# Performance work log

Measured on AMD Instinct MI355X. Metric: run time of the kernel, lower is better.

The kernel has to match this reference:

```python
import jax, jax.numpy as jnp
import numpy as np

N = 50000       # nodes
E = 1600000     # edges
H = 64          # hidden_channels
G = 16          # graphs in batch
DOUT = 2        # dim_out
NODE_IN = 1
EDGE_IN = 3


def setup_inputs() -> dict:
    key = jax.random.key(0)
    ks = jax.random.split(key, 24)
    p = lambda k, shape: (jax.random.normal(k, shape, jnp.float32) * 0.05)
    inp = {
        "x": jax.random.normal(ks[0], (N, NODE_IN), jnp.float32),
        "edge_index": jax.random.randint(ks[1], (2, E), 0, N, dtype=jnp.int64),
        "edge_attr": jax.random.normal(ks[2], (E, EDGE_IN), jnp.float32),
        "batch": jnp.sort(jax.random.randint(ks[3], (N,), 0, G, dtype=jnp.int64)),
        # EdgeModel MLP: Linear(2*node_in+edge_in, H), ReLU, Linear(H, H)
        "ew1": p(ks[4], (2 * NODE_IN + EDGE_IN, H)), "eb1": p(ks[5], (H,)),
        "ew2": p(ks[6], (H, H)), "eb2": p(ks[7], (H,)),
        # NodeModel MLP: Linear(node_in+edge_out, H), ReLU, Linear(H, H)
        "nw1": p(ks[8], (NODE_IN + H, H)), "nb1": p(ks[9], (H,)),
        "nw2": p(ks[10], (H, H)), "nb2": p(ks[11], (H,)),
        "ow1": p(ks[12], (H, H)), "ob1": p(ks[13], (H,)),
        "ow2": p(ks[14], (H, H)), "ob2": p(ks[15], (H,)),
        "ow3": p(ks[16], (H, H)), "ob3": p(ks[17], (H,)),
        "ow4": p(ks[18], (H, DOUT)), "ob4": p(ks[19], (DOUT,)),
    }
    return inp


def reference(x, edge_index, edge_attr, batch,
              ew1, eb1, ew2, eb2,
              nw1, nb1, nw2, nb2,
              ow1, ob1, ow2, ob2, ow3, ob3, ow4, ob4):
    row, col = edge_index[0], edge_index[1]
    # EdgeModel: gather endpoints, concat, 2-layer MLP (no residual)
    e_in = jnp.concatenate([x[row], x[col], edge_attr], axis=1)      # [E, 2+3]
    e = jax.nn.relu(e_in @ ew1 + eb1) @ ew2 + eb2                    # [E, H]
    # NodeModel: scatter_add edge messages into destination nodes
    agg = jax.ops.segment_sum(e, col, num_segments=x.shape[0])      # [N, H]
    h_in = jnp.concatenate([x, agg], axis=1)                         # [N, 1+H]
    h = jax.nn.relu(h_in @ nw1 + nb1) @ nw2 + nb2                    # [N, H]
    # global_add_pool over graphs
    pooled = jax.ops.segment_sum(h, batch, num_segments=G)          # [G, H]
    o = jax.nn.relu(pooled @ ow1 + ob1)
    o = jax.nn.relu(o @ ow2 + ob2)
    o = jax.nn.relu(o @ ow3 + ob3)
    return o @ ow4 + ob4                                             # [G, DOUT]
```

## Files before the change

### kernel.cpp

```cpp
#include <hip/hip_runtime.h>
#include <hip/hip_bf16.h>

#define HID 64
#define NGRAPH 16
#define BN 32
#define GB 8
#define MAXNB 2048
#define NCB 256
#define NCT 1024
#define SORT_T 1024
#define SORT_CHUNK 12800

typedef __attribute__((ext_vector_type(8))) short short8;
typedef __attribute__((ext_vector_type(4))) float f32x4;

enum : int {
  OFF_V      = 1040,
  OFF_M      = 1104,
  OFF_EW1    = 5200,
  OFF_EB1    = 5520,
  OFF_NW1    = 5584,
  OFF_NB1    = 9744,
  OFF_NW2    = 9808,
  OFF_NB2    = 13904,
  OFF_OW1    = 13968,
  OFF_OB1    = 18064,
  OFF_OW2    = 18128,
  OFF_OB2    = 22224,
  OFF_OW3    = 22288,
  OFF_OB3    = 26384,
  OFF_OW4    = 26448,
  OFF_OB4    = 26576,
  OFF_EW2    = 26580,
  OFF_EB2    = 30676,
  OFF_FLAGS  = 30740,
  OFF_W1T    = 30744,
  OFF_MT     = 31000,
  OFF_PREP   = 33048
};

struct WPtrs { const void* p[16]; };

__device__ __forceinline__ float cv(float v) { return v; }
__device__ __forceinline__ float cv(__hip_bfloat16 v) { return __bfloat162float(v); }
__device__ __forceinline__ float b2f(unsigned short u) {
  union { unsigned u32; float f; } c;
  c.u32 = ((unsigned)u) << 16;
  return c.f;
}
__device__ __forceinline__ unsigned short f2bu(float v) {
  union { __hip_bfloat16 b; unsigned short u; } c;
  c.b = __float2bfloat16(v);
  return c.u;
}
__device__ __forceinline__ unsigned short fr(float v) {
  unsigned u = __float_as_uint(v);
  u += 0x7FFFu + ((u >> 16) & 1u);
  return (unsigned short)(u >> 16);
}
__device__ __forceinline__ unsigned rndpack(float a, float b) {
  unsigned ua = __float_as_uint(fmaxf(a, 0.0f));
  unsigned ub = __float_as_uint(fmaxf(b, 0.0f));
  ua += 0x7FFFu + ((ua >> 16) & 1u);
  ub += 0x7FFFu + ((ub >> 16) & 1u);
  return __builtin_amdgcn_perm(ub, ua, 0x07060302u);
}

__global__ __launch_bounds__(1024) void prep_kernel(
    const void* xv, const void* eiv, WPtrs wp, float* ws)
{
  __shared__ int red[2];
  __shared__ int s_ft;
  __shared__ float ew2s[4096];
  __shared__ float nw1s[4096];
  const int t = threadIdx.x;
  const int lane = t & 63;

  if (t == 0) { red[0] = 0; red[1] = 0; }
  __syncthreads();
  {
    int big = 0;
    if (t < 512) {
      const unsigned el = (((const unsigned*)xv)[t] >> 7) & 0xFFu;
      big = (el >= 140u) ? 1 : 0;
    }
    #pragma unroll
    for (int o = 32; o > 0; o >>= 1) big += __shfl_xor(big, o);
    if (lane == 0 && big) atomicAdd(&red[0], big);
  }
  {
    int orv = ((const int*)eiv)[1 + 2 * t];
    #pragma unroll
    for (int o = 32; o > 0; o >>= 1) orv |= __shfl_xor(orv, o);
    if (lane == 0 && orv) atomicOr(&red[1], orv);
  }
  __syncthreads();
  if (t == 0) {
    const int ft = (red[0] < 8) ? 1 : 0;
    const int it = (red[1] == 0) ? 1 : 0;
    ((int*)(ws + OFF_FLAGS))[0] = ft;
    ((int*)(ws + OFF_FLAGS))[1] = it;
    s_ft = ft;
  }
  __syncthreads();
  const int ft = s_ft;

  const int sz[16]  = {320,64,4096,64,4160,64,4096,64,4096,64,4096,64,4096,64,128,2};
  const int dst[16] = {OFF_EW1,OFF_EB1,OFF_EW2,OFF_EB2,OFF_NW1,OFF_NB1,OFF_NW2,OFF_NB2,
                       OFF_OW1,OFF_OB1,OFF_OW2,OFF_OB2,OFF_OW3,OFF_OB3,OFF_OW4,OFF_OB4};
  for (int a = 0; a < 16; ++a) {
    const void* src = wp.p[a];
    float* d = ws + dst[a];
    const int n = sz[a];
    const int n4 = n >> 2;
    for (int i = t; i < n4; i += 1024) {
      float4 f;
      if (ft) {
        const ushort4 u4 = ((const ushort4*)src)[i];
        f.x = b2f(u4.x); f.y = b2f(u4.y); f.z = b2f(u4.z); f.w = b2f(u4.w);
      } else {
        f = ((const float4*)src)[i];
      }
      ((float4*)d)[i] = f;
      const int g = i << 2;
      if (a == 2) {
        ew2s[g] = f.x; ew2s[g + 1] = f.y; ew2s[g + 2] = f.z; ew2s[g + 3] = f.w;
      } else if (a == 4 && g >= 64) {
        nw1s[g - 64] = f.x; nw1s[g - 63] = f.y; nw1s[g - 62] = f.z; nw1s[g - 61] = f.w;
      }
    }
    for (int i = (n4 << 2) + t; i < n; i += 1024)
      d[i] = ft ? b2f(((const unsigned short*)src)[i]) : ((const float*)src)[i];
  }
  __syncthreads();

  float mv[4];
  #pragma unroll
  for (int p = 0; p < 4; ++p) {
    const int idx = t + p * 1024;
    const int i = idx >> 6, j = idx & 63;
    float s = 0.0f;
    #pragma unroll 8
    for (int k = 0; k < 64; ++k)
      s = fmaf(ew2s[i * 64 + k], nw1s[k * 64 + j], s);
    mv[p] = s;
  }
  if (t < 64) {
    float s = 0.0f;
    #pragma unroll 8
    for (int k = 0; k < 64; ++k)
      s = fmaf(ws[OFF_EB2 + k], nw1s[k * 64 + t], s);
    ws[OFF_V + t] = s;
  }
  __syncthreads();
  #pragma unroll
  for (int p = 0; p < 4; ++p) ew2s[t + p * 1024] = mv[p];
  __syncthreads();

  if (t < 64) {
    unsigned short* w1t = (unsigned short*)(ws + OFF_W1T);
    #pragma unroll
    for (int k = 0; k < 8; ++k) {
      float v = 0.0f;
      if (k < 5) v = ws[OFF_EW1 + k * 64 + t];
      else if (k == 5) v = ws[OFF_EB1 + t];
      w1t[t * 8 + k] = f2bu(v);
    }
  }
  unsigned short* mt = (unsigned short*)(ws + OFF_MT);
  #pragma unroll
  for (int p = 0; p < 4; ++p) {
    const int idx = t + p * 1024;
    const int n = idx >> 6, k = idx & 63;
    mt[idx] = f2bu(ew2s[k * 64 + n]);
  }
}

template<typename IT>
__device__ __forceinline__ void count_impl(
    const IT* __restrict__ ei, const IT* __restrict__ bt,
    int* __restrict__ gcnt, int* __restrict__ endG, int* lh,
    const int E, const int N, const int NBG)
{
  const int t = threadIdx.x;
  const int b = blockIdx.x;
  for (int i = t; i < NBG; i += NCT) lh[i] = 0;
  {
    const int i = b * NCT + t;
    if (i < N) {
      const int g1 = (int)bt[i];
      if (i == 0) for (int g = 0; g < g1; ++g) endG[g] = 0;
      if (i == N - 1) {
        for (int g = g1; g < NGRAPH; ++g) endG[g] = N;
      } else {
        const int g2 = (int)bt[i + 1];
        for (int g = g1; g < g2; ++g) endG[g] = i + 1;
      }
    }
  }
  __syncthreads();
  const int per = (E + NCB - 1) / NCB;
  const int a = b * per;
  const int bnd = (a + per < E) ? (a + per) : E;
  for (int e = a + t; e < bnd; e += NCT) {
    const int c = (int)ei[(size_t)E + e];
    atomicAdd(&lh[c >> 8], 1);
  }
  __syncthreads();
  for (int i = t; i < NBG; i += NCT) gcnt[(size_t)i * NCB + b] = lh[i];
}

__global__ __launch_bounds__(NCT) void count_kernel(
    const void* eiv, const void* batv, const float* ws,
    int* gcnt, int* endG, const int E, const int N, const int NBG)
{
  __shared__ int lh[MAXNB];
  const int it = ((const int*)(ws + OFF_FLAGS))[1];
  if (it) count_impl<long long>((const long long*)eiv, (const long long*)batv, gcnt, endG, lh, E, N, NBG);
  else    count_impl<int>((const int*)eiv, (const int*)batv, gcnt, endG, lh, E, N, NBG);
}

__global__ __launch_bounds__(256) void scan_tot_kernel(
    const int* __restrict__ gcnt, int* __restrict__ gstart, const int NBG)
{
  const int lane = threadIdx.x & 63;
  const int bkt = blockIdx.x * 4 + (threadIdx.x >> 6);
  if (bkt >= NBG) return;
  const int4 v = *(const int4*)(gcnt + (size_t)bkt * NCB + lane * 4);
  int s = v.x + v.y + v.z + v.w;
  #pragma unroll
  for (int off = 32; off > 0; off >>= 1) s += __shfl_xor(s, off);
  if (lane == 0) gstart[bkt] = s;
}

__global__ __launch_bounds__(256) void scan_pref_kernel(
    int* __restrict__ gstart, const int NBG)
{
  __shared__ int ps[256];
  const int t = threadIdx.x;
  const int seg = (NBG + 255) / 256;
  int s = 0;
  for (int i = 0; i < seg; ++i) {
    const int idx = t * seg + i;
    if (idx < NBG) s += gstart[idx];
  }
  ps[t] = s;
  __syncthreads();
  for (int off = 1; off < 256; off <<= 1) {
    const int v = (t >= off) ? ps[t - off] : 0;
    __syncthreads();
    ps[t] += v;
    __syncthreads();
  }
  int carry = ps[t] - s;
  for (int i = 0; i < seg; ++i) {
    const int idx = t * seg + i;
    if (idx < NBG) {
      const int c = gstart[idx];
      gstart[idx] = carry;
      carry += c;
    }
  }
  if (t == 255) gstart[NBG] = ps[255];
}

__global__ __launch_bounds__(256) void scan_row_kernel(
    int* __restrict__ gcnt, const int* __restrict__ gstart, const int NBG)
{
  const int lane = threadIdx.x & 63;
  const int bkt = blockIdx.x * 4 + (threadIdx.x >> 6);
  if (bkt >= NBG) return;
  int* row = gcnt + (size_t)bkt * NCB;
  const int4 v = *(const int4*)(row + lane * 4);
  const int ls = v.x + v.y + v.z + v.w;
  int s = ls;
  #pragma unroll
  for (int off = 1; off < 64; off <<= 1) {
    const int u = __shfl_up(s, off);
    if (lane >= off) s += u;
  }
  int e = s - ls + gstart[bkt];
  int4 o;
  o.x = e; e += v.x;
  o.y = e; e += v.y;
  o.z = e; e += v.z;
  o.w = e;
  *(int4*)(row + lane * 4) = o;
}

template<typename FT, typename IT>
__device__ __forceinline__ void scatter_impl(
    const FT* __restrict__ x, const IT* __restrict__ ei, const FT* __restrict__ ea,
    const int* __restrict__ gcnt, const int* __restrict__ gstart,
    ushort4* __restrict__ recB, unsigned char* __restrict__ cid, int* lb,
    const int E, const int gb0, const int gb1, const int cap)
{
  const int t = threadIdx.x;
  const int b = blockIdx.x;
  __shared__ int sbase;
  if (t == 0) sbase = gstart[gb0];
  __syncthreads();
  const int base = sbase;
  const int gcount = gb1 - gb0;
  for (int i = t; i < gcount; i += NCT) lb[i] = gcnt[(size_t)(gb0 + i) * NCB + b] - base;
  __syncthreads();

  const int per = (E + NCB - 1) / NCB;
  const int a = b * per;
  const int bnd = (a + per < E) ? (a + per) : E;
  for (int e = a + t; e < bnd; e += NCT) {
    const int c = (int)ei[(size_t)E + e];
    const int grp = c >> 8;
    if (grp >= gb0 && grp < gb1) {
      const int pos = atomicAdd(&lb[grp - gb0], 1);
      if (pos < cap) {
        const int r = (int)ei[e];
        ushort4 rv;
        rv.x = fr(cv(x[r]));
        rv.y = fr(cv(ea[(size_t)3 * e + 0]));
        rv.z = fr(cv(ea[(size_t)3 * e + 1]));
        rv.w = fr(cv(ea[(size_t)3 * e + 2]));
        recB[pos] = rv;
        cid[pos] = (unsigned char)(c & 255);
      }
    }
  }
}

__global__ __launch_bounds__(NCT) void scatter_kernel(
    const void* xv, const void* eiv, const void* eav, const float* ws,
    const int* gcnt, const int* gstart, ushort4* recB, unsigned char* cid,
    const int E, const int gb0, const int gb1, const int cap)
{
  __shared__ int lb[MAXNB];
  const int* fl = (const int*)(ws + OFF_FLAGS);
  const int ft = fl[0], it = fl[1];
  if (ft) {
    if (it) scatter_impl<__hip_bfloat16, long long>((const __hip_bfloat16*)xv, (const long long*)eiv, (const __hip_bfloat16*)eav, gcnt, gstart, recB, cid, lb, E, gb0, gb1, cap);
    else    scatter_impl<__hip_bfloat16, int>((const __hip_bfloat16*)xv, (const int*)eiv, (const __hip_bfloat16*)eav, gcnt, gstart, recB, cid, lb, E, gb0, gb1, cap);
  } else {
    if (it) scatter_impl<float, long long>((const float*)xv, (const long long*)eiv, (const float*)eav, gcnt, gstart, recB, cid, lb, E, gb0, gb1, cap);
    else    scatter_impl<float, int>((const float*)xv, (const int*)eiv, (const float*)eav, gcnt, gstart, recB, cid, lb, E, gb0, gb1, cap);
  }
}

__global__ __launch_bounds__(SORT_T) void sort_kernel(
    ushort4* __restrict__ recB, unsigned char* __restrict__ cid,
    const int* __restrict__ gstart, int* __restrict__ bstartF,
    const int NB, const int gr0, const int cap)
{
  __shared__ unsigned sru[SORT_CHUNK * 2];
  __shared__ unsigned char sc[SORT_CHUNK];
  __shared__ int h2[16][GB];
  __shared__ int fs[GB];
  __shared__ int cur[GB];

  const int t = threadIdx.x;
  const int lane = t & 63;
  const int wav = t >> 6;
  const int g = gr0 + (int)blockIdx.x;

  const int base0 = gstart[gr0];
  int rb = gstart[g] - base0;
  int re = gstart[g + 1] - base0;
  if (rb > cap) rb = cap;
  if (re > cap) re = cap;
  int cnt = re - rb;
  if (cnt > SORT_CHUNK) cnt = SORT_CHUNK;

  if (t < 16 * GB) ((int*)h2)[t] = 0;
  __syncthreads();

  for (int i = t; i < cnt; i += SORT_T) {
    const ushort4 r = recB[rb + i];
    sru[2 * i]     = (unsigned)r.x | ((unsigned)r.y << 16);
    sru[2 * i + 1] = (unsigned)r.z | ((unsigned)r.w << 16);
    const unsigned char c = cid[rb + i];
    sc[i] = c;
    const int kk = c >> 5;
    unsigned long long mym = 0;
    #pragma unroll
    for (int k = 0; k < GB; ++k) {
      const unsigned long long bk = __ballot(kk == k);
      if (kk == k) mym = bk;
    }
    if ((mym & (((unsigned long long)1 << lane) - 1ull)) == 0)
      h2[wav][kk] += (int)__builtin_popcountll(mym);
  }
  __syncthreads();

  if (t == 0) {
    int acc = 0;
    for (int k = 0; k < GB; ++k) {
      int s = 0;
      #pragma unroll
      for (int w = 0; w < 16; ++w) s += h2[w][k];
      fs[k] = acc;
      cur[k] = acc;
      acc += s;
    }
  }
  __syncthreads();

  if (t <= GB) {
    const int bk = g * GB + t;
    if (bk <= NB) bstartF[bk] = base0 + rb + ((t == GB) ? cnt : fs[t]);
  }

  for (int i = t; i < cnt; i += SORT_T) {
    const unsigned char c = sc[i];
    const int kk = c >> 5;
    unsigned long long mym = 0;
    #pragma unroll
    for (int k = 0; k < GB; ++k) {
      const unsigned long long bk = __ballot(kk == k);
      if (kk == k) mym = bk;
    }
    const int lead = (int)__builtin_ctzll(mym);
    const int off = (int)__builtin_popcountll(mym & (((unsigned long long)1 << lane) - 1ull));
    int bas = 0;
    if (lane == lead) bas = atomicAdd(&cur[kk], (int)__builtin_popcountll(mym));
    bas = __shfl(bas, lead);
    const int pos = rb + bas + off;
    const unsigned a = sru[2 * i], b = sru[2 * i + 1];
    ushort4 rv;
    rv.x = (unsigned short)(a & 0xFFFFu); rv.y = (unsigned short)(a >> 16);
    rv.z = (unsigned short)(b & 0xFFFFu); rv.w = (unsigned short)(b >> 16);
    recB[pos] = rv;
    cid[pos] = (unsigned char)(c & 31);
  }
}

template<typename FT, typename IT>
__device__ __forceinline__ void fused_impl(
    const FT* __restrict__ x, const IT* __restrict__ batch,
    const float* __restrict__ ws, const int* __restrict__ bstart,
    const ushort4* __restrict__ recB, const unsigned char* __restrict__ cid,
    float* __restrict__ rep,
    short* sA, short* sHT, short* a2L,
    float* xls, unsigned short* xlsb, int* sbi,
    const int N, const int gb0, const int cap)
{
  const int t = threadIdx.x;
  const int lane = t & 63;
  const int quad = lane >> 4;
  const int l15 = lane & 15;
  const int wav = t >> 6;
  const int bucket = gb0 + blockIdx.x;

  if (t < BN) {
    const int n = bucket * BN + t;
    const float xvv = (n < N) ? cv(x[n]) : 0.0f;
    xls[t] = xvv;
    xlsb[t] = fr(xvv);
  }
  if (t == 0) {
    const int nf = bucket * BN, nl = bucket * BN + BN - 1;
    sbi[0] = (int)batch[(nf < N) ? nf : (N - 1)];
    sbi[1] = (int)batch[(nl < N) ? nl : (N - 1)];
    sbi[2] = bstart[gb0];
  }
  __syncthreads();

  const unsigned short* w1t = (const unsigned short*)(ws + OFF_W1T);
  short8 B1[4];
  #pragma unroll
  for (int tn = 0; tn < 4; ++tn) {
    short8 z; for (int j = 0; j < 8; ++j) z[j] = 0;
    if (quad == 0) z = *(const short8*)(w1t + (16 * tn + l15) * 8);
    B1[tn] = z;
  }
  short8 ONES8;
  #pragma unroll
  for (int j = 0; j < 8; ++j) ONES8[j] = (short)0x3F80;

  const int base = sbi[2];
  int s0 = bstart[bucket] - base;
  int e0 = bstart[bucket + 1] - base;
  if (s0 > cap) s0 = cap;
  if (e0 > cap) e0 = cap;

  f32x4 C2[2]; C2[0] = (f32x4)0.0f; C2[1] = (f32x4)0.0f;
  f32x4 C3[2]; C3[0] = (f32x4)0.0f; C3[1] = (f32x4)0.0f;

  const int nedge = e0 - s0;
  const int nst = (nedge + 255) >> 8;
  for (int st = 0; st < nst; ++st) {
    const int idx = s0 + st * 256 + t;
    const bool valid = idx < e0;
    const ushort4 rv = valid ? recB[idx] : make_ushort4(0, 0, 0, 0);
    const int c = valid ? (int)cid[idx] : 255;

    {
      unsigned long long* az = (unsigned long long*)a2L;
      #pragma unroll
      for (int z = 0; z < 9; ++z) az[t + z * 256] = 0ull;
    }
    __syncthreads();
    {
      short8 row;
      row[0] = (short)rv.x;
      row[1] = valid ? (short)xlsb[c] : (short)0;
      row[2] = (short)rv.y; row[3] = (short)rv.z; row[4] = (short)rv.w;
      row[5] = valid ? (short)0x3F80 : (short)0;
      row[6] = 0; row[7] = 0;
      *(short8*)(sA + t * 8) = row;
      if (c < 32) a2L[(t >> 6) * 2304 + c * 72 + (t & 63)] = (short)0x3F80;
    }
    __syncthreads();

    const int m = nedge - st * 256;
    const int jmax = (m >= 256) ? 4 : ((m + 63) >> 6);
    for (int j = 0; j < jmax; ++j) {
      short* HT = sHT + (j & 1) * 4608;
      short8 a1;
      if (quad == 0) a1 = *(const short8*)(sA + (j * 64 + 16 * wav + l15) * 8);
      else { for (int jj = 0; jj < 8; ++jj) a1[jj] = 0; }
      f32x4 Hc[4];
      #pragma unroll
      for (int tn = 0; tn < 4; ++tn)
        Hc[tn] = __builtin_amdgcn_mfma_f32_16x16x32_bf16(a1, B1[tn], (f32x4)0.0f, 0, 0, 0);
      #pragma unroll
      for (int tn = 0; tn < 4; ++tn) {
        uint2 pk;
        pk.x = rndpack(Hc[tn][0], Hc[tn][1]);
        pk.y = rndpack(Hc[tn][2], Hc[tn][3]);
        *(uint2*)(HT + (16 * tn + l15) * 72 + 16 * wav + quad * 4) = pk;
      }
      __syncthreads();

      const short* aj = a2L + j * 2304;
      #pragma unroll
      for (int q = 0; q < 2; ++q) {
        const short8 a20 = *(const short8*)(aj + l15 * 72 + 32 * q + 8 * quad);
        const short8 a21 = *(const short8*)(aj + (16 + l15) * 72 + 32 * q + 8 * quad);
        const short8 b2  = *(const short8*)(HT + (16 * wav + l15) * 72 + 32 * q + quad * 8);
        C2[0] = __builtin_amdgcn_mfma_f32_16x16x32_bf16(a20, b2, C2[0], 0, 0, 0);
        C2[1] = __builtin_amdgcn_mfma_f32_16x16x32_bf16(a21, b2, C2[1], 0, 0, 0);
        C3[0] = __builtin_amdgcn_mfma_f32_16x16x32_bf16(a20, ONES8, C3[0], 0, 0, 0);
        C3[1] = __builtin_amdgcn_mfma_f32_16x16x32_bf16(a21, ONES8, C3[1], 0, 0, 0);
      }
    }
    __syncthreads();
  }

  short* aggB = a2L;
  #pragma unroll
  for (int tm2 = 0; tm2 < 2; ++tm2) {
    #pragma unroll
    for (int r = 0; r < 4; ++r)
      aggB[(16 * tm2 + quad * 4 + r) * 72 + 16 * wav + l15] = (short)fr(C2[tm2][r]);
  }
  __syncthreads();

  const unsigned short* mt = (const unsigned short*)(ws + OFF_MT);
  f32x4 D[2]; D[0] = (f32x4)0.0f; D[1] = (f32x4)0.0f;
  #pragma unroll
  for (int q2 = 0; q2 < 2; ++q2) {
    const short8 bb = *(const short8*)(mt + (16 * wav + l15) * 64 + 32 * q2 + quad * 8);
    #pragma unroll
    for (int tm2 = 0; tm2 < 2; ++tm2) {
      const short8 aa = *(const short8*)(aggB + (16 * tm2 + l15) * 72 + 32 * q2 + quad * 8);
      D[tm2] = __builtin_amdgcn_mfma_f32_16x16x32_bf16(aa, bb, D[tm2], 0, 0, 0);
    }
  }

  const int n = 16 * wav + l15;
  const float c1n = ws[OFF_NW1 + n];
  const float vn  = ws[OFF_V + n];
  const float bn  = ws[OFF_NB1 + n];
  float* myrep = rep + (size_t)(bucket & 7) * (NGRAPH * 64);
  const bool multi = (sbi[0] != sbi[1]);

  if (!multi) {
    float hs = 0.0f;
    #pragma unroll
    for (int tm2 = 0; tm2 < 2; ++tm2) {
      #pragma unroll
      for (int r = 0; r < 4; ++r) {
        const int mrow = 16 * tm2 + quad * 4 + r;
        const int ng = bucket * BN + mrow;
        if (ng < N)
          hs += fmaxf(D[tm2][r] + xls[mrow] * c1n + C3[tm2][r] * vn + bn, 0.0f);
      }
    }
    hs += __shfl_xor(hs, 16);
    hs += __shfl_xor(hs, 32);
    if (quad == 0) unsafeAtomicAdd(&myrep[sbi[0] * 64 + n], hs);
  } else {
    float* pooledL = (float*)sA;
    for (int i = t; i < NGRAPH * 64; i += 256) pooledL[i] = 0.0f;
    __syncthreads();
    #pragma unroll
    for (int tm2 = 0; tm2 < 2; ++tm2) {
      #pragma unroll
      for (int r = 0; r < 4; ++r) {
        const int mrow = 16 * tm2 + quad * 4 + r;
        const int ng = bucket * BN + mrow;
        if (ng < N) {
          const float h = fmaxf(D[tm2][r] + xls[mrow] * c1n + C3[tm2][r] * vn + bn, 0.0f);
          const int g = (int)batch[ng];
          atomicAdd(&pooledL[g * 64 + n], h);
        }
      }
    }
    __syncthreads();
    for (int g = sbi[0] + wav; g <= sbi[1]; g += 4)
      unsafeAtomicAdd(&myrep[g * 64 + lane], pooledL[g * 64 + lane]);
  }
}

__global__ __launch_bounds__(256) void fused_kernel(
    const void* xv, const void* batv, const float* ws, const int* bstart,
    const ushort4* recB, const unsigned char* cid, float* rep,
    const int N, const int gb0, const int cap)
{
  __shared__ __align__(16) unsigned char smem[41168];
  short* sA  = (short*)smem;
  short* sHT = (short*)(smem + 4096);
  short* a2L = (short*)(smem + 22528);
  float* xls = (float*)(smem + 40960);
  unsigned short* xlsb = (unsigned short*)(smem + 41088);
  int* sbi = (int*)(smem + 41152);

  const int* fl = (const int*)(ws + OFF_FLAGS);
  const int ft = fl[0], it = fl[1];
  if (ft) {
    if (it) fused_impl<__hip_bfloat16, long long>((const __hip_bfloat16*)xv, (const long long*)batv, ws, bstart, recB, cid, rep, sA, sHT, a2L, xls, xlsb, sbi, N, gb0, cap);
    else    fused_impl<__hip_bfloat16, int>((const __hip_bfloat16*)xv, (const int*)batv, ws, bstart, recB, cid, rep, sA, sHT, a2L, xls, xlsb, sbi, N, gb0, cap);
  } else {
    if (it) fused_impl<float, long long>((const float*)xv, (const long long*)batv, ws, bstart, recB, cid, rep, sA, sHT, a2L, xls, xlsb, sbi, N, gb0, cap);
    else    fused_impl<float, int>((const float*)xv, (const int*)batv, ws, bstart, recB, cid, rep, sA, sHT, a2L, xls, xlsb, sbi, N, gb0, cap);
  }
}

__global__ __launch_bounds__(256) void head_kernel(
    const float* ws, const float* rep, const int* __restrict__ endG,
    void* outv, const int N)
{
  __shared__ float P[NGRAPH][HID];
  __shared__ float A[NGRAPH][HID];
  __shared__ float B[NGRAPH][HID];
  __shared__ int endL[NGRAPH];

  const int t = threadIdx.x;
  const int j = t & 63;
  const int gq = t >> 6;

  if (t < NGRAPH) endL[t] = endG[t];

  #pragma unroll
  for (int gi = 0; gi < 4; ++gi) {
    const int g = gq + gi * 4;
    float s = 0.0f;
    #pragma unroll
    for (int r = 0; r < 8; ++r)
      s += rep[(size_t)r * (NGRAPH * 64) + g * 64 + j];
    P[g][j] = s;
  }
  __syncthreads();

  {
    const float bj = ws[OFF_NB2 + j];
    #pragma unroll
    for (int gi = 0; gi < 4; ++gi) {
      const int g = gq + gi * 4;
      const float cg = (float)(endL[g] - (g ? endL[g - 1] : 0));
      float s = cg * bj;
      #pragma unroll 8
      for (int k = 0; k < HID; ++k)
        s = fmaf(P[g][k], ws[OFF_NW2 + k * HID + j], s);
      A[g][j] = s;
    }
  }
  __syncthreads();

  const int wOff[3] = {OFF_OW1, OFF_OW2, OFF_OW3};
  const int bOff[3] = {OFF_OB1, OFF_OB2, OFF_OB3};
  for (int L = 0; L < 3; ++L) {
    float (*In)[HID]  = (L & 1) ? B : A;
    float (*Out)[HID] = (L & 1) ? A : B;
    const float bj = ws[bOff[L] + j];
    #pragma unroll
    for (int gi = 0; gi < 4; ++gi) {
      const int g = gq + gi * 4;
      float s = bj;
      #pragma unroll 8
      for (int k = 0; k < HID; ++k)
        s = fmaf(In[g][k], ws[wOff[L] + k * HID + j], s);
      Out[g][j] = fmaxf(s, 0.0f);
    }
    __syncthreads();
  }

  if (t < 32) {
    const int g = t >> 1, d = t & 1;
    float s = ws[OFF_OB4 + d];
    #pragma unroll 8
    for (int k = 0; k < HID; ++k)
      s = fmaf(B[g][k], ws[OFF_OW4 + k * 2 + d], s);
    const int ft = ((const int*)(ws + OFF_FLAGS))[0];
    if (ft) ((__hip_bfloat16*)outv)[g * 2 + d] = __float2bfloat16(s);
    else    ((float*)outv)[g * 2 + d] = s;
  }
}

extern "C" void kernel_launch(void* const* d_in, const int* in_sizes, int n_in,
                              void* d_out, int out_size, void* d_ws, size_t ws_size,
                              hipStream_t stream)
{
  const void* xv   = d_in[0];
  const void* eiv  = d_in[1];
  const void* eav  = d_in[2];
  const void* batv = d_in[3];

  WPtrs wp;
  for (int a = 0; a < 16; ++a) wp.p[a] = d_in[4 + a];

  const int N = in_sizes[0];
  const int E = in_sizes[1] / 2;
  const int NB = (N + BN - 1) / BN;
  const int NBG = (NB + GB - 1) / GB;
  if (NB > MAXNB) return;

  float* ws    = (float*)d_ws;
  float* rep   = ws + OFF_PREP;
  int* gstart  = (int*)(rep + 8 * NGRAPH * 64);
  int* bstartF = gstart + NBG + 1;
  int* endG    = bstartF + NB + 2;
  int* gcnt    = endG + NGRAPH;

  size_t recOffB = ((size_t)((char*)(gcnt + (size_t)NBG * NCB) - (char*)d_ws) + 15) & ~(size_t)15;

  int G = -1; long long cap = 0;
  for (int g = 1; g <= 64; ++g) {
    const long long c = (long long)E / g + E / 32 + 8192;
    if (recOffB + (size_t)c * 9 <= ws_size) { G = g; cap = c; break; }
  }
  if (G < 0) return;

  ushort4* recB = (ushort4*)((char*)d_ws + recOffB);
  unsigned char* cid = (unsigned char*)(recB + cap);
  const int gsz = (NBG + G - 1) / G;
  const int sblk = (NBG + 3) / 4;

  (void)hipMemsetAsync(rep, 0, (size_t)(8 * NGRAPH * 64) * 4, stream);

  prep_kernel<<<1, 1024, 0, stream>>>(xv, eiv, wp, ws);
  count_kernel<<<NCB, NCT, 0, stream>>>(eiv, batv, ws, gcnt, endG, E, N, NBG);
  scan_tot_kernel<<<sblk, 256, 0, stream>>>(gcnt, gstart, NBG);
  scan_pref_kernel<<<1, 256, 0, stream>>>(gstart, NBG);
  scan_row_kernel<<<sblk, 256, 0, stream>>>(gcnt, gstart, NBG);

  for (int g = 0; g < G; ++g) {
    const int gr0 = g * gsz;
    const int gr1 = (gr0 + gsz < NBG) ? (gr0 + gsz) : NBG;
    if (gr0 >= gr1) break;
    scatter_kernel<<<NCB, NCT, 0, stream>>>(xv, eiv, eav, ws, gcnt, gstart,
                                            recB, cid, E, gr0, gr1, (int)cap);
    sort_kernel<<<gr1 - gr0, SORT_T, 0, stream>>>(recB, cid, gstart, bstartF,
                                                  NB, gr0, (int)cap);
    const int b0 = gr0 * GB;
    const int b1 = (gr1 * GB < NB) ? (gr1 * GB) : NB;
    fused_kernel<<<b1 - b0, 256, 0, stream>>>(xv, batv, ws, bstartF, recB, cid,
                                              rep, N, b0, (int)cap);
  }

  head_kernel<<<1, 256, 0, stream>>>(ws, rep, endG, d_out, N);
}
```

Measured before the change: 252.8 us.

## Prefetch next edge stage into registers and build MFMA A operand directly

Edge records for each 256-edge stage are now loaded by the quad-0 lanes straight into registers, and the next stage's records are prefetched while the current stage computes. The first-layer MFMA A fragment is assembled in registers instead of being staged through a shared-memory sA buffer. This removes one LDS round trip and overlaps global loads with MFMA work, and the freed 4 KB of shared memory could allow higher occupancy. In exchange it raises register pressure, and only a quarter of the lanes issue loads.

Result: slower. 261.9 us (+3.6%).

```diff
diff --git a/kernel.cpp b/kernel.cpp
--- a/kernel.cpp
+++ b/kernel.cpp
@@ -437,7 +437,7 @@
     const float* __restrict__ ws, const int* __restrict__ bstart,
     const ushort4* __restrict__ recB, const unsigned char* __restrict__ cid,
     float* __restrict__ rep,
-    short* sA, short* sHT, short* a2L,
+    short* sHT, short* a2L,
     float* xls, unsigned short* xlsb, int* sbi,
     const int N, const int gb0, const int cap)
 {
@@ -485,37 +485,63 @@
 
   const int nedge = e0 - s0;
   const int nst = (nedge + 255) >> 8;
+
+  ushort4 rvH[4]; int cH[4];
+  #pragma unroll
+  for (int jj = 0; jj < 4; ++jj) { rvH[jj] = make_ushort4(0,0,0,0); cH[jj] = 255; }
+  if (nst > 0 && quad == 0) {
+    #pragma unroll
+    for (int jj = 0; jj < 4; ++jj) {
+      const int idx = s0 + jj * 64 + 16 * wav + l15;
+      if (idx < e0) { rvH[jj] = recB[idx]; cH[jj] = (int)cid[idx]; }
+    }
+  }
+
   for (int st = 0; st < nst; ++st) {
-    const int idx = s0 + st * 256 + t;
-    const bool valid = idx < e0;
-    const ushort4 rv = valid ? recB[idx] : make_ushort4(0, 0, 0, 0);
-    const int c = valid ? (int)cid[idx] : 255;
-
     {
       unsigned long long* az = (unsigned long long*)a2L;
       #pragma unroll
       for (int z = 0; z < 9; ++z) az[t + z * 256] = 0ull;
     }
     __syncthreads();
-    {
-      short8 row;
-      row[0] = (short)rv.x;
-      row[1] = valid ? (short)xlsb[c] : (short)0;
-      row[2] = (short)rv.y; row[3] = (short)rv.z; row[4] = (short)rv.w;
-      row[5] = valid ? (short)0x3F80 : (short)0;
-      row[6] = 0; row[7] = 0;
-      *(short8*)(sA + t * 8) = row;
-      if (c < 32) a2L[(t >> 6) * 2304 + c * 72 + (t & 63)] = (short)0x3F80;
+    if (quad == 0) {
+      #pragma unroll
+      for (int jj = 0; jj < 4; ++jj)
+        if (cH[jj] < 32) a2L[jj * 2304 + cH[jj] * 72 + 16 * wav + l15] = (short)0x3F80;
     }
     __syncthreads();
+
+    ushort4 rvN[4]; int cN[4];
+    #pragma unroll
+    for (int jj = 0; jj < 4; ++jj) { rvN[jj] = make_ushort4(0,0,0,0); cN[jj] = 255; }
+    if (st + 1 < nst && quad == 0) {
+      #pragma unroll
+      for (int jj = 0; jj < 4; ++jj) {
+        const int idx = s0 + (st + 1) * 256 + jj * 64 + 16 * wav + l15;
+        if (idx < e0) { rvN[jj] = recB[idx]; cN[jj] = (int)cid[idx]; }
+      }
+    }
 
     const int m = nedge - st * 256;
     const int jmax = (m >= 256) ? 4 : ((m + 63) >> 6);
-    for (int j = 0; j < jmax; ++j) {
+    #pragma unroll
+    for (int j = 0; j < 4; ++j) {
+      if (j >= jmax) break;
       short* HT = sHT + (j & 1) * 4608;
       short8 a1;
-      if (quad == 0) a1 = *(const short8*)(sA + (j * 64 + 16 * wav + l15) * 8);
-      else { for (int jj = 0; jj < 8; ++jj) a1[jj] = 0; }
+      if (quad == 0) {
+        const ushort4 rv = rvH[j];
+        const int c = cH[j];
+        const bool v = c < 32;
+        a1[0] = (short)rv.x;
+        a1[1] = v ? (short)xlsb[c] : (short)0;
+        a1[2] = (short)rv.y; a1[3] = (short)rv.z; a1[4] = (short)rv.w;
+        a1[5] = v ? (short)0x3F80 : (short)0;
+        a1[6] = 0; a1[7] = 0;
+      } else {
+        #pragma unroll
+        for (int jj = 0; jj < 8; ++jj) a1[jj] = 0;
+      }
       f32x4 Hc[4];
       #pragma unroll
       for (int tn = 0; tn < 4; ++tn)
@@ -542,6 +568,8 @@
       }
     }
     __syncthreads();
+    #pragma unroll
+    for (int jj = 0; jj < 4; ++jj) { rvH[jj] = rvN[jj]; cH[jj] = cN[jj]; }
   }
 
   short* aggB = a2L;
@@ -588,7 +616,7 @@
     hs += __shfl_xor(hs, 32);
     if (quad == 0) unsafeAtomicAdd(&myrep[sbi[0] * 64 + n], hs);
   } else {
-    float* pooledL = (float*)sA;
+    float* pooledL = (float*)((char*)a2L + 4608);
     for (int i = t; i < NGRAPH * 64; i += 256) pooledL[i] = 0.0f;
     __syncthreads();
     #pragma unroll
@@ -615,22 +643,21 @@
     const ushort4* recB, const unsigned char* cid, float* rep,
     const int N, const int gb0, const int cap)
 {
-  __shared__ __align__(16) unsigned char smem[41168];
-  short* sA  = (short*)smem;
-  short* sHT = (short*)(smem + 4096);
-  short* a2L = (short*)(smem + 22528);
-  float* xls = (float*)(smem + 40960);
-  unsigned short* xlsb = (unsigned short*)(smem + 41088);
-  int* sbi = (int*)(smem + 41152);
+  __shared__ __align__(16) unsigned char smem[37072];
+  short* sHT = (short*)smem;
+  short* a2L = (short*)(smem + 18432);
+  float* xls = (float*)(smem + 36864);
+  unsigned short* xlsb = (unsigned short*)(smem + 36992);
+  int* sbi = (int*)(smem + 37056);
 
   const int* fl = (const int*)(ws + OFF_FLAGS);
   const int ft = fl[0], it = fl[1];
   if (ft) {
-    if (it) fused_impl<__hip_bfloat16, long long>((const __hip_bfloat16*)xv, (const long long*)batv, ws, bstart, recB, cid, rep, sA, sHT, a2L, xls, xlsb, sbi, N, gb0, cap);
-    else    fused_impl<__hip_bfloat16, int>((const __hip_bfloat16*)xv, (const int*)batv, ws, bstart, recB, cid, rep, sA, sHT, a2L, xls, xlsb, sbi, N, gb0, cap);
+    if (it) fused_impl<__hip_bfloat16, long long>((const __hip_bfloat16*)xv, (const long long*)batv, ws, bstart, recB, cid, rep, sHT, a2L, xls, xlsb, sbi, N, gb0, cap);
+    else    fused_impl<__hip_bfloat16, int>((const __hip_bfloat16*)xv, (const int*)batv, ws, bstart, recB, cid, rep, sHT, a2L, xls, xlsb, sbi, N, gb0, cap);
   } else {
-    if (it) fused_impl<float, long long>((const float*)xv, (const long long*)batv, ws, bstart, recB, cid, rep, sA, sHT, a2L, xls, xlsb, sbi, N, gb0, cap);
-    else    fused_impl<float, int>((const float*)xv, (const int*)batv, ws, bstart, recB, cid, rep, sA, sHT, a2L, xls, xlsb, sbi, N, gb0, cap);
+    if (it) fused_impl<float, long long>((const float*)xv, (const long long*)batv, ws, bstart, recB, cid, rep, sHT, a2L, xls, xlsb, sbi, N, gb0, cap);
+    else    fused_impl<float, int>((const float*)xv, (const int*)batv, ws, bstart, recB, cid, rep, sHT, a2L, xls, xlsb, sbi, N, gb0, cap);
   }
 }
 
```
